# Optimization experiments

Measured on AMD Instinct MI355X. Metric: run time of the kernel, lower is better.

The kernel has to match this reference:

```python
import jax, jax.numpy as jnp
import numpy as np

BN_EPS = 1e-5


def setup_inputs() -> dict:
    key = jax.random.key(0)
    ks = jax.random.split(key, 8)
    N, Cin, Cout, D, H, W = 4, 512, 256, 256, 128, 128
    feat_ffm = jax.random.normal(ks[0], (N, Cin, H, W), dtype=jnp.float32)
    coarse_x = jax.random.normal(ks[1], (N, D, H, W), dtype=jnp.float32)
    # conv1: 1x1, no bias; BN (eval mode: running stats); conv2: 1x1 with bias
    w1 = jax.random.normal(ks[2], (Cout, Cin), dtype=jnp.float32) * (1.0 / np.sqrt(Cin))
    bn_gamma = jnp.ones((Cout,), dtype=jnp.float32)
    bn_beta = jnp.zeros((Cout,), dtype=jnp.float32)
    bn_mean = jax.random.normal(ks[3], (Cout,), dtype=jnp.float32) * 0.1
    bn_var = jax.random.uniform(ks[4], (Cout,), dtype=jnp.float32, minval=0.5, maxval=1.5)
    w2 = jax.random.normal(ks[5], (Cout, Cout), dtype=jnp.float32) * (1.0 / np.sqrt(Cout))
    b2 = jnp.zeros((Cout,), dtype=jnp.float32)
    return {"feat_ffm": feat_ffm, "coarse_x": coarse_x, "w1": w1,
            "bn_gamma": bn_gamma, "bn_beta": bn_beta, "bn_mean": bn_mean,
            "bn_var": bn_var, "w2": w2, "b2": b2}


def reference(feat_ffm, coarse_x, w1, bn_gamma, bn_beta, bn_mean, bn_var, w2, b2):
    N, D, H, W = coarse_x.shape
    # conv1 (1x1) + BN(eval) + ReLU; Dropout2d is identity in eval mode
    x = jnp.einsum('nihw,oi->nohw', feat_ffm, w1)
    scale = bn_gamma * jax.lax.rsqrt(bn_var + BN_EPS)
    x = x * scale[None, :, None, None] + (bn_beta - bn_mean * scale)[None, :, None, None]
    x = jax.nn.relu(x)  # [N, C, H, W]
    C = x.shape[1]
    q = coarse_x.reshape(N, D, H * W)          # proj_query / proj_value
    k = x.reshape(N, C, H * W)                 # proj_key (pre-permute)
    energy = jnp.einsum('nds,ncs->ndc', q, k)  # [N, D, C]
    energy_new = jnp.max(energy, axis=-1, keepdims=True) - energy
    attention = jax.nn.softmax(energy_new, axis=-1)        # [N, D, C]
    out = jnp.einsum('ndc,nds->ncs', attention, q)         # attention^T @ value
    out = out.reshape(N, C, H, W)
    out = jnp.einsum('nchw,oc->nohw', out, w2) + b2[None, :, None, None]
    return out
```

## Files before the change

kernel.cpp:

```cpp
#include <hip/hip_runtime.h>


#define S_DIM 16384
#define C_DIM 256
#define CIN 512

typedef unsigned short u16;
typedef __attribute__((ext_vector_type(8))) short bf16x8;
typedef __attribute__((ext_vector_type(4))) float f32x4;

__device__ __forceinline__ u16 f2bf(float x) {
    unsigned u = __float_as_uint(x);
    u += 0x7fff + ((u >> 16) & 1);
    return (u16)(u >> 16);
}
__device__ __forceinline__ float bf2f(u16 h) {
    return __uint_as_float(((unsigned)h) << 16);
}
__device__ __forceinline__ void gld16(const u16* g, u16* l) {
    __builtin_amdgcn_global_load_lds((const __attribute__((address_space(1))) void*)g,
                                     (__attribute__((address_space(3))) void*)l, 16, 0, 0);
}

__global__ __launch_bounds__(256) void prep_kernel(
    const float* __restrict__ feat, const float* __restrict__ coarse,
    const float* __restrict__ w1, const float* __restrict__ gamma,
    const float* __restrict__ beta, const float* __restrict__ mean,
    const float* __restrict__ var,
    u16* __restrict__ fThi, u16* __restrict__ fTlo,
    u16* __restrict__ qhi, u16* __restrict__ qlo,
    u16* __restrict__ w1hi, u16* __restrict__ w1lo, float* __restrict__ b1) {
    __shared__ u16 Th[64][65], Tl[64][65];
    int b = blockIdx.x;
    int t = threadIdx.x;
    if (b < 8192) {
        int s0 = (b & 255) * 64;
        int i0 = ((b >> 8) & 7) * 64;
        size_t sb = (size_t)(b >> 11) * 8388608;
#pragma unroll
        for (int p = 0; p < 4; ++p) {
            int idx = t + p * 256;
            int row = idx >> 4, c4 = (idx & 15) * 4;
            float4 v = *(const float4*)&feat[sb + (size_t)(i0 + row) * S_DIM + s0 + c4];
            float vv[4] = {v.x, v.y, v.z, v.w};
#pragma unroll
            for (int j = 0; j < 4; ++j) {
                u16 h = f2bf(vv[j]);
                Th[c4 + j][row] = h;
                Tl[c4 + j][row] = f2bf(vv[j] - bf2f(h));
            }
        }
        __syncthreads();
#pragma unroll
        for (int p = 0; p < 2; ++p) {
            int idx = t + p * 256;
            int row = idx >> 3, c8 = (idx & 7) * 8;
            u16 hh[8], ll[8];
#pragma unroll
            for (int j = 0; j < 8; ++j) { hh[j] = Th[row][c8 + j]; ll[j] = Tl[row][c8 + j]; }
            *(uint4*)&fThi[sb + (size_t)(s0 + row) * CIN + i0 + c8] = *(uint4*)hh;
            *(uint4*)&fTlo[sb + (size_t)(s0 + row) * CIN + i0 + c8] = *(uint4*)ll;
        }
    } else if (b < 12288) {
        size_t i = (size_t)(b - 8192) * 256 + t;
        for (size_t c = i; c < 4194304u; c += 1048576u) {
            float4 v = ((const float4*)coarse)[c];
            float vv[4] = {v.x, v.y, v.z, v.w};
            u16 h[4], l[4];
#pragma unroll
            for (int j = 0; j < 4; ++j) {
                h[j] = f2bf(vv[j]);
                l[j] = f2bf(vv[j] - bf2f(h[j]));
            }
            *(uint2*)&qhi[c * 4] = *(uint2*)h;
            *(uint2*)&qlo[c * 4] = *(uint2*)l;
        }
    } else {
        int o = (b - 12288) * 16 + (t >> 4);
        int lane16 = t & 15;
        float sc = gamma[o] * rsqrtf(var[o] + 1e-5f);
        for (int i = lane16; i < CIN; i += 16) {
            float v = w1[o * CIN + i] * sc;
            u16 h = f2bf(v);
            w1hi[o * CIN + i] = h;
            w1lo[o * CIN + i] = f2bf(v - bf2f(h));
        }
        if (lane16 == 0) b1[o] = beta[o] - mean[o] * sc;
    }
}

template <int SPLIT, int EPI>
__global__ __launch_bounds__(256) void gemm_nt(
    const u16* __restrict__ Ah, const u16* __restrict__ Al, long aStride,
    const u16* __restrict__ Bh, const u16* __restrict__ Bl, long bStride,
    int K, int kLen,
    const float* __restrict__ bias,
    float* __restrict__ outF, long oStrideF,
    u16* __restrict__ oHi, u16* __restrict__ oLo, long oStrideH,
    int ldOut) {
    __shared__ u16 AhS[4096];
    __shared__ u16 BhS[4096];
    __shared__ u16 AlS[SPLIT == 3 ? 4096 : 8];
    __shared__ u16 BlS[SPLIT == 3 ? 4096 : 8];

    int m0, n0, kBeg;
    if (EPI == 0) {
        kBeg = blockIdx.x * kLen;
        m0 = (blockIdx.y >> 1) * 128;
        n0 = (blockIdx.y & 1) * 128;
    } else {
        kBeg = 0;
        n0 = blockIdx.x * 128;
        m0 = blockIdx.y * 128;
    }
    int bz = blockIdx.z;
    int tid = threadIdx.x;
    int wave = tid >> 6, lane = tid & 63;

    int c0 = wave * 128 + lane;
    int c1 = c0 + 64;
    int r0 = c0 >> 2, k0 = (c0 & 3) * 8;
    int r1 = c1 >> 2, k1 = (c1 & 3) * 8;
    const u16* gAh0 = Ah + (size_t)bz * aStride + (size_t)(m0 + r0) * K + kBeg + k0;
    const u16* gAh1 = Ah + (size_t)bz * aStride + (size_t)(m0 + r1) * K + kBeg + k1;
    const u16* gBh0 = Bh + (size_t)bz * bStride + (size_t)(n0 + r0) * K + kBeg + k0;
    const u16* gBh1 = Bh + (size_t)bz * bStride + (size_t)(n0 + r1) * K + kBeg + k1;
    const u16 *gAl0 = nullptr, *gAl1 = nullptr, *gBl0 = nullptr, *gBl1 = nullptr;
    if (SPLIT == 3) {
        gAl0 = Al + (size_t)bz * aStride + (size_t)(m0 + r0) * K + kBeg + k0;
        gAl1 = Al + (size_t)bz * aStride + (size_t)(m0 + r1) * K + kBeg + k1;
        gBl0 = Bl + (size_t)bz * bStride + (size_t)(n0 + r0) * K + kBeg + k0;
        gBl1 = Bl + (size_t)bz * bStride + (size_t)(n0 + r1) * K + kBeg + k1;
    }

    int quad = lane >> 4, l15 = lane & 15;
    int wm = wave >> 1, wn = wave & 1;
    int aBase = (wm * 64 + l15) * 32 + quad * 8;
    int bBase = (wn * 64 + l15) * 32 + quad * 8;

    f32x4 zero = {0.f, 0.f, 0.f, 0.f};
    f32x4 acc[4][4];
#pragma unroll
    for (int i = 0; i < 4; ++i)
#pragma unroll
        for (int j = 0; j < 4; ++j) acc[i][j] = zero;

    for (int kb = 0; kb < kLen; kb += 32) {
        __syncthreads();
        gld16(gAh0, AhS + c0 * 8);
        gld16(gAh1, AhS + c1 * 8);
        gld16(gBh0, BhS + c0 * 8);
        gld16(gBh1, BhS + c1 * 8);
        gAh0 += 32; gAh1 += 32; gBh0 += 32; gBh1 += 32;
        if (SPLIT == 3) {
            gld16(gAl0, AlS + c0 * 8);
            gld16(gAl1, AlS + c1 * 8);
            gld16(gBl0, BlS + c0 * 8);
            gld16(gBl1, BlS + c1 * 8);
            gAl0 += 32; gAl1 += 32; gBl0 += 32; gBl1 += 32;
        }
        __syncthreads();

        bf16x8 a_h[4], b_h[4], a_l[4], b_l[4];
#pragma unroll
        for (int t = 0; t < 4; ++t) {
            a_h[t] = *(const bf16x8*)&AhS[aBase + t * 512];
            b_h[t] = *(const bf16x8*)&BhS[bBase + t * 512];
            if (SPLIT == 3) {
                a_l[t] = *(const bf16x8*)&AlS[aBase + t * 512];
                b_l[t] = *(const bf16x8*)&BlS[bBase + t * 512];
            }
        }
#pragma unroll
        for (int mt = 0; mt < 4; ++mt)
#pragma unroll
            for (int nt = 0; nt < 4; ++nt) {
                acc[mt][nt] = __builtin_amdgcn_mfma_f32_16x16x32_bf16(a_h[mt], b_h[nt], acc[mt][nt], 0, 0, 0);
                if (SPLIT == 3) {
                    acc[mt][nt] = __builtin_amdgcn_mfma_f32_16x16x32_bf16(a_h[mt], b_l[nt], acc[mt][nt], 0, 0, 0);
                    acc[mt][nt] = __builtin_amdgcn_mfma_f32_16x16x32_bf16(a_l[mt], b_h[nt], acc[mt][nt], 0, 0, 0);
                }
            }
    }

    float* Ce = nullptr;
    if (EPI == 0) Ce = outF + ((size_t)(blockIdx.x * gridDim.z + bz)) * 65536;
#pragma unroll
    for (int mt = 0; mt < 4; ++mt) {
#pragma unroll
        for (int r = 0; r < 4; ++r) {
            int row = m0 + wm * 64 + mt * 16 + quad * 4 + r;
            float bi = (EPI != 0) ? bias[row] : 0.f;
#pragma unroll
            for (int nt = 0; nt < 4; ++nt) {
                int cc = n0 + wn * 64 + nt * 16 + l15;
                float v = acc[mt][nt][r];
                if (EPI == 0) {
                    Ce[(size_t)row * ldOut + cc] = v;
                } else if (EPI == 1) {
                    v = fmaxf(v + bi, 0.f);
                    u16 h = f2bf(v);
                    size_t o = (size_t)bz * oStrideH + (size_t)row * ldOut + cc;
                    oHi[o] = h;
                    oLo[o] = f2bf(v - bf2f(h));
                } else {
                    outF[(size_t)bz * oStrideF + (size_t)row * ldOut + cc] = v + bi;
                }
            }
        }
    }
}

__global__ __launch_bounds__(256) void post_kernel(const float* __restrict__ Ep,
                                                   float* __restrict__ att,
                                                   const u16* __restrict__ qhi,
                                                   u16* __restrict__ qT) {
    __shared__ u16 T[64][65];
    __shared__ float red[4], red2[4];
    int b = blockIdx.x;
    int t = threadIdx.x;
    if (b < 1024) {
        int n = b >> 8, d = b & 255;
        const float* p = Ep + ((size_t)n * 256 + d) * 256 + t;
        float v = 0.f;
#pragma unroll 8
        for (int s = 0; s < 32; ++s) v += p[(size_t)s * 262144];
        float m = v;
#pragma unroll
        for (int o = 32; o > 0; o >>= 1) m = fminf(m, __shfl_xor(m, o, 64));
        int lane = t & 63, wid = t >> 6;
        if (lane == 0) red[wid] = m;
        __syncthreads();
        m = fminf(fminf(red[0], red[1]), fminf(red[2], red[3]));
        float e = expf(m - v);
        float s = e;
#pragma unroll
        for (int o = 32; o > 0; o >>= 1) s += __shfl_xor(s, o, 64);
        if (lane == 0) red2[wid] = s;
        __syncthreads();
        s = red2[0] + red2[1] + red2[2] + red2[3];
        att[(size_t)b * 256 + t] = e / s;
    } else {
        int i = b - 1024;
        int s0 = (i & 255) * 64;
        int d0 = ((i >> 8) & 3) * 64;
        size_t sb = (size_t)(i >> 10) * 4194304;
#pragma unroll
        for (int p = 0; p < 2; ++p) {
            int idx = t + p * 256;
            int row = idx >> 3, c8 = (idx & 7) * 8;
            u16 v[8];
            *(uint4*)v = *(const uint4*)&qhi[sb + (size_t)(d0 + row) * S_DIM + s0 + c8];
#pragma unroll
            for (int j = 0; j < 8; ++j) T[c8 + j][row] = v[j];
        }
        __syncthreads();
#pragma unroll
        for (int p = 0; p < 2; ++p) {
            int idx = t + p * 256;
            int row = idx >> 3, c8 = (idx & 7) * 8;
            u16 v[8];
#pragma unroll
            for (int j = 0; j < 8; ++j) v[j] = T[row][c8 + j];
            *(uint4*)&qT[sb + (size_t)(s0 + row) * C_DIM + d0 + c8] = *(uint4*)v;
        }
    }
}

__global__ __launch_bounds__(256) void m2h_kernel(const float* __restrict__ w2,
                                                  const float* __restrict__ att,
                                                  u16* __restrict__ M2h) {
    int t = blockIdx.x * 256 + threadIdx.x;
    int d = t & 255, o = (t >> 8) & 255, n = t >> 16;
    const float4* wr = (const float4*)(w2 + (size_t)o * C_DIM);
    const float4* ar = (const float4*)(att + ((size_t)n * C_DIM + d) * C_DIM);
    float s = 0.0f;
#pragma unroll 4
    for (int c4 = 0; c4 < 64; ++c4) {
        float4 w = wr[c4];
        float4 a = ar[c4];
        s += w.x * a.x + w.y * a.y + w.z * a.z + w.w * a.w;
    }
    M2h[((size_t)n * C_DIM + o) * C_DIM + d] = f2bf(s);
}

extern "C" void kernel_launch(void* const* d_in, const int* in_sizes, int n_in,
                              void* d_out, int out_size, void* d_ws, size_t ws_size,
                              hipStream_t stream) {
    const float* feat   = (const float*)d_in[0];
    const float* coarse = (const float*)d_in[1];
    const float* w1     = (const float*)d_in[2];
    const float* gamma  = (const float*)d_in[3];
    const float* beta   = (const float*)d_in[4];
    const float* mean   = (const float*)d_in[5];
    const float* var    = (const float*)d_in[6];
    const float* w2     = (const float*)d_in[7];
    const float* b2     = (const float*)d_in[8];
    float* out = (float*)d_out;

    char* base = (char*)d_ws;
    u16* qhi   = (u16*)(base);
    u16* qlo   = (u16*)(base + 33554432);
    u16* khi   = (u16*)(base + 67108864);
    u16* klo   = (u16*)(base + 100663296);
    u16* fThi  = (u16*)(base + 134217728);
    u16* fTlo  = (u16*)(base + 201326592);
    u16* qT    = (u16*)(base + 268435456);
    float* Ep  = (float*)(base + 301989888);
    float* att = (float*)(base + 335544320);
    u16* M2h   = (u16*)(base + 336592896);
    u16* w1hi  = (u16*)(base + 337117184);
    u16* w1lo  = (u16*)(base + 337379328);
    float* b1  = (float*)(base + 337641472);

    prep_kernel<<<12304, 256, 0, stream>>>(feat, coarse, w1, gamma, beta, mean, var,
                                           fThi, fTlo, qhi, qlo, w1hi, w1lo, b1);

    gemm_nt<3, 1><<<dim3(128, 2, 4), 256, 0, stream>>>(
        w1hi, w1lo, 0, fThi, fTlo, 8388608, CIN, CIN, b1,
        nullptr, 0, khi, klo, 4194304, S_DIM);

    gemm_nt<3, 0><<<dim3(32, 4, 4), 256, 0, stream>>>(
        qhi, qlo, 4194304, khi, klo, 4194304, S_DIM, 512, nullptr,
        Ep, 65536, nullptr, nullptr, 0, C_DIM);

    post_kernel<<<5120, 256, 0, stream>>>(Ep, att, qhi, qT);

    m2h_kernel<<<1024, 256, 0, stream>>>(w2, att, M2h);

    gemm_nt<1, 2><<<dim3(128, 2, 4), 256, 0, stream>>>(
        M2h, nullptr, 65536, qT, nullptr, 4194304, C_DIM, C_DIM, b2,
        out, 4194304, nullptr, nullptr, 0, S_DIM);
}
```

Baseline: 496.2 us.

## Fuse fp32 transpose/split conversion into conv and final GEMM loads

```diff
diff --git a/kernel.cpp b/kernel.cpp
--- a/kernel.cpp
+++ b/kernel.cpp
@@ -21,48 +21,21 @@
     __builtin_amdgcn_global_load_lds((const __attribute__((address_space(1))) void*)g,
                                      (__attribute__((address_space(3))) void*)l, 16, 0, 0);
 }
+__device__ __forceinline__ void gld4(const float* g, float* l) {
+    __builtin_amdgcn_global_load_lds((const __attribute__((address_space(1))) void*)g,
+                                     (__attribute__((address_space(3))) void*)l, 4, 0, 0);
+}
 
 __global__ __launch_bounds__(256) void prep_kernel(
-    const float* __restrict__ feat, const float* __restrict__ coarse,
-    const float* __restrict__ w1, const float* __restrict__ gamma,
-    const float* __restrict__ beta, const float* __restrict__ mean,
-    const float* __restrict__ var,
-    u16* __restrict__ fThi, u16* __restrict__ fTlo,
+    const float* __restrict__ coarse, const float* __restrict__ w1,
+    const float* __restrict__ gamma, const float* __restrict__ beta,
+    const float* __restrict__ mean, const float* __restrict__ var,
     u16* __restrict__ qhi, u16* __restrict__ qlo,
     u16* __restrict__ w1hi, u16* __restrict__ w1lo, float* __restrict__ b1) {
-    __shared__ u16 Th[64][65], Tl[64][65];
     int b = blockIdx.x;
     int t = threadIdx.x;
-    if (b < 8192) {
-        int s0 = (b & 255) * 64;
-        int i0 = ((b >> 8) & 7) * 64;
-        size_t sb = (size_t)(b >> 11) * 8388608;
-#pragma unroll
-        for (int p = 0; p < 4; ++p) {
-            int idx = t + p * 256;
-            int row = idx >> 4, c4 = (idx & 15) * 4;
-            float4 v = *(const float4*)&feat[sb + (size_t)(i0 + row) * S_DIM + s0 + c4];
-            float vv[4] = {v.x, v.y, v.z, v.w};
-#pragma unroll
-            for (int j = 0; j < 4; ++j) {
-                u16 h = f2bf(vv[j]);
-                Th[c4 + j][row] = h;
-                Tl[c4 + j][row] = f2bf(vv[j] - bf2f(h));
-            }
-        }
-        __syncthreads();
-#pragma unroll
-        for (int p = 0; p < 2; ++p) {
-            int idx = t + p * 256;
-            int row = idx >> 3, c8 = (idx & 7) * 8;
-            u16 hh[8], ll[8];
-#pragma unroll
-            for (int j = 0; j < 8; ++j) { hh[j] = Th[row][c8 + j]; ll[j] = Tl[row][c8 + j]; }
-            *(uint4*)&fThi[sb + (size_t)(s0 + row) * CIN + i0 + c8] = *(uint4*)hh;
-            *(uint4*)&fTlo[sb + (size_t)(s0 + row) * CIN + i0 + c8] = *(uint4*)ll;
-        }
-    } else if (b < 12288) {
-        size_t i = (size_t)(b - 8192) * 256 + t;
+    if (b < 4096) {
+        size_t i = (size_t)b * 256 + t;
         for (size_t c = i; c < 4194304u; c += 1048576u) {
             float4 v = ((const float4*)coarse)[c];
             float vv[4] = {v.x, v.y, v.z, v.w};
@@ -76,7 +49,7 @@
             *(uint2*)&qlo[c * 4] = *(uint2*)l;
         }
     } else {
-        int o = (b - 12288) * 16 + (t >> 4);
+        int o = (b - 4096) * 16 + (t >> 4);
         int lane16 = t & 15;
         float sc = gamma[o] * rsqrtf(var[o] + 1e-5f);
         for (int i = lane16; i < CIN; i += 16) {
@@ -89,49 +62,125 @@
     }
 }
 
-template <int SPLIT, int EPI>
-__global__ __launch_bounds__(256) void gemm_nt(
-    const u16* __restrict__ Ah, const u16* __restrict__ Al, long aStride,
-    const u16* __restrict__ Bh, const u16* __restrict__ Bl, long bStride,
-    int K, int kLen,
-    const float* __restrict__ bias,
-    float* __restrict__ outF, long oStrideF,
-    u16* __restrict__ oHi, u16* __restrict__ oLo, long oStrideH,
-    int ldOut) {
-    __shared__ u16 AhS[4096];
-    __shared__ u16 BhS[4096];
-    __shared__ u16 AlS[SPLIT == 3 ? 4096 : 8];
-    __shared__ u16 BlS[SPLIT == 3 ? 4096 : 8];
-
-    int m0, n0, kBeg;
-    if (EPI == 0) {
-        kBeg = blockIdx.x * kLen;
-        m0 = (blockIdx.y >> 1) * 128;
-        n0 = (blockIdx.y & 1) * 128;
-    } else {
-        kBeg = 0;
-        n0 = blockIdx.x * 128;
-        m0 = blockIdx.y * 128;
-    }
+__global__ __launch_bounds__(256) void conv_kernel(
+    const u16* __restrict__ w1hi, const u16* __restrict__ w1lo,
+    const float* __restrict__ feat, const float* __restrict__ b1,
+    u16* __restrict__ khi, u16* __restrict__ klo) {
+    __shared__ u16 AhS[4096], AlS[4096];
+    __shared__ float BfS[32 * 133];
+    int s0 = blockIdx.x * 128;
+    int m0 = blockIdx.y * 128;
     int bz = blockIdx.z;
-    int tid = threadIdx.x;
-    int wave = tid >> 6, lane = tid & 63;
-
-    int c0 = wave * 128 + lane;
-    int c1 = c0 + 64;
+    int tid = threadIdx.x, wave = tid >> 6, lane = tid & 63;
+
+    int c0 = wave * 128 + lane, c1 = c0 + 64;
     int r0 = c0 >> 2, k0 = (c0 & 3) * 8;
     int r1 = c1 >> 2, k1 = (c1 & 3) * 8;
-    const u16* gAh0 = Ah + (size_t)bz * aStride + (size_t)(m0 + r0) * K + kBeg + k0;
-    const u16* gAh1 = Ah + (size_t)bz * aStride + (size_t)(m0 + r1) * K + kBeg + k1;
-    const u16* gBh0 = Bh + (size_t)bz * bStride + (size_t)(n0 + r0) * K + kBeg + k0;
-    const u16* gBh1 = Bh + (size_t)bz * bStride + (size_t)(n0 + r1) * K + kBeg + k1;
-    const u16 *gAl0 = nullptr, *gAl1 = nullptr, *gBl0 = nullptr, *gBl1 = nullptr;
-    if (SPLIT == 3) {
-        gAl0 = Al + (size_t)bz * aStride + (size_t)(m0 + r0) * K + kBeg + k0;
-        gAl1 = Al + (size_t)bz * aStride + (size_t)(m0 + r1) * K + kBeg + k1;
-        gBl0 = Bl + (size_t)bz * bStride + (size_t)(n0 + r0) * K + kBeg + k0;
-        gBl1 = Bl + (size_t)bz * bStride + (size_t)(n0 + r1) * K + kBeg + k1;
-    }
+    const u16* gA0h = w1hi + (size_t)(m0 + r0) * CIN + k0;
+    const u16* gA1h = w1hi + (size_t)(m0 + r1) * CIN + k1;
+    const u16* gA0l = w1lo + (size_t)(m0 + r0) * CIN + k0;
+    const u16* gA1l = w1lo + (size_t)(m0 + r1) * CIN + k1;
+    const float* fB = feat + (size_t)bz * ((size_t)CIN * S_DIM) + s0 + lane;
+
+    int quad = lane >> 4, l15 = lane & 15;
+    int wm = wave >> 1, wn = wave & 1;
+    int aBase = (wm * 64 + l15) * 32 + quad * 8;
+
+    f32x4 zero = {0.f, 0.f, 0.f, 0.f};
+    f32x4 acc[4][4];
+#pragma unroll
+    for (int i = 0; i < 4; ++i)
+#pragma unroll
+        for (int j = 0; j < 4; ++j) acc[i][j] = zero;
+
+    for (int kb = 0; kb < CIN; kb += 32) {
+        __syncthreads();
+        gld16(gA0h, AhS + c0 * 8);
+        gld16(gA1h, AhS + c1 * 8);
+        gld16(gA0l, AlS + c0 * 8);
+        gld16(gA1l, AlS + c1 * 8);
+        gA0h += 32; gA1h += 32; gA0l += 32; gA1l += 32;
+#pragma unroll
+        for (int j = 0; j < 16; ++j) {
+            int cc = wave * 16 + j;
+            int i = cc >> 1, h = cc & 1;
+            gld4(fB + (size_t)(kb + i) * S_DIM + h * 64, BfS + i * 133 + h * 64 + lane);
+        }
+        __syncthreads();
+
+        bf16x8 a_h[4], a_l[4];
+#pragma unroll
+        for (int t = 0; t < 4; ++t) {
+            a_h[t] = *(const bf16x8*)&AhS[aBase + t * 512];
+            a_l[t] = *(const bf16x8*)&AlS[aBase + t * 512];
+        }
+        bf16x8 b_h[4], b_l[4];
+#pragma unroll
+        for (int nt = 0; nt < 4; ++nt) {
+            int n = wn * 64 + nt * 16 + l15;
+            union { u16 u[8]; bf16x8 v; } th, tl;
+#pragma unroll
+            for (int j = 0; j < 8; ++j) {
+                float f = BfS[(quad * 8 + j) * 133 + n];
+                u16 h = f2bf(f);
+                th.u[j] = h;
+                tl.u[j] = (u16)(__float_as_uint(f - bf2f(h)) >> 16);
+            }
+            b_h[nt] = th.v;
+            b_l[nt] = tl.v;
+        }
+#pragma unroll
+        for (int mt = 0; mt < 4; ++mt)
+#pragma unroll
+            for (int nt = 0; nt < 4; ++nt) {
+                acc[mt][nt] = __builtin_amdgcn_mfma_f32_16x16x32_bf16(a_h[mt], b_h[nt], acc[mt][nt], 0, 0, 0);
+                acc[mt][nt] = __builtin_amdgcn_mfma_f32_16x16x32_bf16(a_h[mt], b_l[nt], acc[mt][nt], 0, 0, 0);
+                acc[mt][nt] = __builtin_amdgcn_mfma_f32_16x16x32_bf16(a_l[mt], b_h[nt], acc[mt][nt], 0, 0, 0);
+            }
+    }
+
+#pragma unroll
+    for (int mt = 0; mt < 4; ++mt) {
+#pragma unroll
+        for (int r = 0; r < 4; ++r) {
+            int row = m0 + wm * 64 + mt * 16 + quad * 4 + r;
+            float bi = b1[row];
+#pragma unroll
+            for (int nt = 0; nt < 4; ++nt) {
+                int cc = s0 + wn * 64 + nt * 16 + l15;
+                float v = fmaxf(acc[mt][nt][r] + bi, 0.f);
+                u16 h = f2bf(v);
+                size_t o = (size_t)bz * 4194304 + (size_t)row * S_DIM + cc;
+                khi[o] = h;
+                klo[o] = f2bf(v - bf2f(h));
+            }
+        }
+    }
+}
+
+__global__ __launch_bounds__(256) void energy_kernel(
+    const u16* __restrict__ qhi, const u16* __restrict__ qlo,
+    const u16* __restrict__ khi, const u16* __restrict__ klo,
+    float* __restrict__ Ep) {
+    __shared__ u16 AhS[4096], BhS[4096], AlS[4096], BlS[4096];
+    int kBeg = blockIdx.x * 256;
+    int m0 = (blockIdx.y >> 1) * 128;
+    int n0 = (blockIdx.y & 1) * 128;
+    int bz = blockIdx.z;
+    int tid = threadIdx.x, wave = tid >> 6, lane = tid & 63;
+
+    int c0 = wave * 128 + lane, c1 = c0 + 64;
+    int r0 = c0 >> 2, k0 = (c0 & 3) * 8;
+    int r1 = c1 >> 2, k1 = (c1 & 3) * 8;
+    size_t bo = (size_t)bz * 4194304;
+    const u16* gA0h = qhi + bo + (size_t)(m0 + r0) * S_DIM + kBeg + k0;
+    const u16* gA1h = qhi + bo + (size_t)(m0 + r1) * S_DIM + kBeg + k1;
+    const u16* gB0h = khi + bo + (size_t)(n0 + r0) * S_DIM + kBeg + k0;
+    const u16* gB1h = khi + bo + (size_t)(n0 + r1) * S_DIM + kBeg + k1;
+    const u16* gA0l = qlo + bo + (size_t)(m0 + r0) * S_DIM + kBeg + k0;
+    const u16* gA1l = qlo + bo + (size_t)(m0 + r1) * S_DIM + kBeg + k1;
+    const u16* gB0l = klo + bo + (size_t)(n0 + r0) * S_DIM + kBeg + k0;
+    const u16* gB1l = klo + bo + (size_t)(n0 + r1) * S_DIM + kBeg + k1;
 
     int quad = lane >> 4, l15 = lane & 15;
     int wm = wave >> 1, wn = wave & 1;
@@ -145,20 +194,18 @@
 #pragma unroll
         for (int j = 0; j < 4; ++j) acc[i][j] = zero;
 
-    for (int kb = 0; kb < kLen; kb += 32) {
-        __syncthreads();
-        gld16(gAh0, AhS + c0 * 8);
-        gld16(gAh1, AhS + c1 * 8);
-        gld16(gBh0, BhS + c0 * 8);
-        gld16(gBh1, BhS + c1 * 8);
-        gAh0 += 32; gAh1 += 32; gBh0 += 32; gBh1 += 32;
-        if (SPLIT == 3) {
-            gld16(gAl0, AlS + c0 * 8);
-            gld16(gAl1, AlS + c1 * 8);
-            gld16(gBl0, BlS + c0 * 8);
-            gld16(gBl1, BlS + c1 * 8);
-            gAl0 += 32; gAl1 += 32; gBl0 += 32; gBl1 += 32;
-        }
+    for (int kb = 0; kb < 256; kb += 32) {
+        __syncthreads();
+        gld16(gA0h, AhS + c0 * 8);
+        gld16(gA1h, AhS + c1 * 8);
+        gld16(gB0h, BhS + c0 * 8);
+        gld16(gB1h, BhS + c1 * 8);
+        gld16(gA0l, AlS + c0 * 8);
+        gld16(gA1l, AlS + c1 * 8);
+        gld16(gB0l, BlS + c0 * 8);
+        gld16(gB1l, BlS + c1 * 8);
+        gA0h += 32; gA1h += 32; gB0h += 32; gB1h += 32;
+        gA0l += 32; gA1l += 32; gB0l += 32; gB1l += 32;
         __syncthreads();
 
         bf16x8 a_h[4], b_h[4], a_l[4], b_l[4];
@@ -166,105 +213,57 @@
         for (int t = 0; t < 4; ++t) {
             a_h[t] = *(const bf16x8*)&AhS[aBase + t * 512];
             b_h[t] = *(const bf16x8*)&BhS[bBase + t * 512];
-            if (SPLIT == 3) {
-                a_l[t] = *(const bf16x8*)&AlS[aBase + t * 512];
-                b_l[t] = *(const bf16x8*)&BlS[bBase + t * 512];
-            }
+            a_l[t] = *(const bf16x8*)&AlS[aBase + t * 512];
+            b_l[t] = *(const bf16x8*)&BlS[bBase + t * 512];
         }
 #pragma unroll
         for (int mt = 0; mt < 4; ++mt)
 #pragma unroll
             for (int nt = 0; nt < 4; ++nt) {
                 acc[mt][nt] = __builtin_amdgcn_mfma_f32_16x16x32_bf16(a_h[mt], b_h[nt], acc[mt][nt], 0, 0, 0);
-                if (SPLIT == 3) {
-                    acc[mt][nt] = __builtin_amdgcn_mfma_f32_16x16x32_bf16(a_h[mt], b_l[nt], acc[mt][nt], 0, 0, 0);
-                    acc[mt][nt] = __builtin_amdgcn_mfma_f32_16x16x32_bf16(a_l[mt], b_h[nt], acc[mt][nt], 0, 0, 0);
-                }
-            }
-    }
-
-    float* Ce = nullptr;
-    if (EPI == 0) Ce = outF + ((size_t)(blockIdx.x * gridDim.z + bz)) * 65536;
-#pragma unroll
-    for (int mt = 0; mt < 4; ++mt) {
+                acc[mt][nt] = __builtin_amdgcn_mfma_f32_16x16x32_bf16(a_h[mt], b_l[nt], acc[mt][nt], 0, 0, 0);
+                acc[mt][nt] = __builtin_amdgcn_mfma_f32_16x16x32_bf16(a_l[mt], b_h[nt], acc[mt][nt], 0, 0, 0);
+            }
+    }
+
+    float* Ce = Ep + ((size_t)(blockIdx.x * 4 + bz)) * 65536;
+#pragma unroll
+    for (int mt = 0; mt < 4; ++mt)
 #pragma unroll
         for (int r = 0; r < 4; ++r) {
             int row = m0 + wm * 64 + mt * 16 + quad * 4 + r;
-            float bi = (EPI != 0) ? bias[row] : 0.f;
 #pragma unroll
             for (int nt = 0; nt < 4; ++nt) {
                 int cc = n0 + wn * 64 + nt * 16 + l15;
-                float v = acc[mt][nt][r];
-                if (EPI == 0) {
-                    Ce[(size_t)row * ldOut + cc] = v;
-                } else if (EPI == 1) {
-                    v = fmaxf(v + bi, 0.f);
-                    u16 h = f2bf(v);
-                    size_t o = (size_t)bz * oStrideH + (size_t)row * ldOut + cc;
-                    oHi[o] = h;
-                    oLo[o] = f2bf(v - bf2f(h));
-                } else {
-                    outF[(size_t)bz * oStrideF + (size_t)row * ldOut + cc] = v + bi;
-                }
-            }
-        }
-    }
-}
-
-__global__ __launch_bounds__(256) void post_kernel(const float* __restrict__ Ep,
-                                                   float* __restrict__ att,
-                                                   const u16* __restrict__ qhi,
-                                                   u16* __restrict__ qT) {
-    __shared__ u16 T[64][65];
+                Ce[(size_t)row * C_DIM + cc] = acc[mt][nt][r];
+            }
+        }
+}
+
+__global__ __launch_bounds__(256) void softmax_kernel(const float* __restrict__ Ep,
+                                                      float* __restrict__ att) {
     __shared__ float red[4], red2[4];
     int b = blockIdx.x;
     int t = threadIdx.x;
-    if (b < 1024) {
-        int n = b >> 8, d = b & 255;
-        const float* p = Ep + ((size_t)n * 256 + d) * 256 + t;
-        float v = 0.f;
+    const float* p = Ep + (size_t)b * 256 + t;
+    float v = 0.f;
 #pragma unroll 8
-        for (int s = 0; s < 32; ++s) v += p[(size_t)s * 262144];
-        float m = v;
-#pragma unroll
-        for (int o = 32; o > 0; o >>= 1) m = fminf(m, __shfl_xor(m, o, 64));
-        int lane = t & 63, wid = t >> 6;
-        if (lane == 0) red[wid] = m;
-        __syncthreads();
-        m = fminf(fminf(red[0], red[1]), fminf(red[2], red[3]));
-        float e = expf(m - v);
-        float s = e;
-#pragma unroll
-        for (int o = 32; o > 0; o >>= 1) s += __shfl_xor(s, o, 64);
-        if (lane == 0) red2[wid] = s;
-        __syncthreads();
-        s = red2[0] + red2[1] + red2[2] + red2[3];
-        att[(size_t)b * 256 + t] = e / s;
-    } else {
-        int i = b - 1024;
-        int s0 = (i & 255) * 64;
-        int d0 = ((i >> 8) & 3) * 64;
-        size_t sb = (size_t)(i >> 10) * 4194304;
-#pragma unroll
-        for (int p = 0; p < 2; ++p) {
-            int idx = t + p * 256;
-            int row = idx >> 3, c8 = (idx & 7) * 8;
-            u16 v[8];
-            *(uint4*)v = *(const uint4*)&qhi[sb + (size_t)(d0 + row) * S_DIM + s0 + c8];
-#pragma unroll
-            for (int j = 0; j < 8; ++j) T[c8 + j][row] = v[j];
-        }
-        __syncthreads();
-#pragma unroll
-        for (int p = 0; p < 2; ++p) {
-            int idx = t + p * 256;
-            int row = idx >> 3, c8 = (idx & 7) * 8;
-            u16 v[8];
-#pragma unroll
-            for (int j = 0; j < 8; ++j) v[j] = T[row][c8 + j];
-            *(uint4*)&qT[sb + (size_t)(s0 + row) * C_DIM + d0 + c8] = *(uint4*)v;
-        }
-    }
+    for (int s = 0; s < 64; ++s) v += p[(size_t)s * 262144];
+    float m = v;
+#pragma unroll
+    for (int o = 32; o > 0; o >>= 1) m = fminf(m, __shfl_xor(m, o, 64));
+    int lane = t & 63, wid = t >> 6;
+    if (lane == 0) red[wid] = m;
+    __syncthreads();
+    m = fminf(fminf(red[0], red[1]), fminf(red[2], red[3]));
+    float e = expf(m - v);
+    float s = e;
+#pragma unroll
+    for (int o = 32; o > 0; o >>= 1) s += __shfl_xor(s, o, 64);
+    if (lane == 0) red2[wid] = s;
+    __syncthreads();
+    s = red2[0] + red2[1] + red2[2] + red2[3];
+    att[(size_t)b * 256 + t] = e / s;
 }
 
 __global__ __launch_bounds__(256) void m2h_kernel(const float* __restrict__ w2,
@@ -284,6 +283,80 @@
     M2h[((size_t)n * C_DIM + o) * C_DIM + d] = f2bf(s);
 }
 
+__global__ __launch_bounds__(256) void final_kernel(
+    const u16* __restrict__ M2h, const float* __restrict__ coarse,
+    const float* __restrict__ b2, float* __restrict__ out) {
+    __shared__ u16 AhS[4096];
+    __shared__ float BfS[32 * 133];
+    int s0 = blockIdx.x * 128;
+    int m0 = blockIdx.y * 128;
+    int bz = blockIdx.z;
+    int tid = threadIdx.x, wave = tid >> 6, lane = tid & 63;
+
+    int c0 = wave * 128 + lane, c1 = c0 + 64;
+    int r0 = c0 >> 2, k0 = (c0 & 3) * 8;
+    int r1 = c1 >> 2, k1 = (c1 & 3) * 8;
+    const u16* gA0 = M2h + (size_t)bz * 65536 + (size_t)(m0 + r0) * C_DIM + k0;
+    const u16* gA1 = M2h + (size_t)bz * 65536 + (size_t)(m0 + r1) * C_DIM + k1;
+    const float* fB = coarse + (size_t)bz * 4194304 + s0 + lane;
+
+    int quad = lane >> 4, l15 = lane & 15;
+    int wm = wave >> 1, wn = wave & 1;
+    int aBase = (wm * 64 + l15) * 32 + quad * 8;
+
+    f32x4 zero = {0.f, 0.f, 0.f, 0.f};
+    f32x4 acc[4][4];
+#pragma unroll
+    for (int i = 0; i < 4; ++i)
+#pragma unroll
+        for (int j = 0; j < 4; ++j) acc[i][j] = zero;
+
+    for (int kb = 0; kb < C_DIM; kb += 32) {
+        __syncthreads();
+        gld16(gA0, AhS + c0 * 8);
+        gld16(gA1, AhS + c1 * 8);
+        gA0 += 32; gA1 += 32;
+#pragma unroll
+        for (int j = 0; j < 16; ++j) {
+            int cc = wave * 16 + j;
+            int i = cc >> 1, h = cc & 1;
+            gld4(fB + (size_t)(kb + i) * S_DIM + h * 64, BfS + i * 133 + h * 64 + lane);
+        }
+        __syncthreads();
+
+        bf16x8 a_h[4];
+#pragma unroll
+        for (int t = 0; t < 4; ++t) a_h[t] = *(const bf16x8*)&AhS[aBase + t * 512];
+        bf16x8 b_h[4];
+#pragma unroll
+        for (int nt = 0; nt < 4; ++nt) {
+            int n = wn * 64 + nt * 16 + l15;
+            union { u16 u[8]; bf16x8 v; } th;
+#pragma unroll
+            for (int j = 0; j < 8; ++j) th.u[j] = f2bf(BfS[(quad * 8 + j) * 133 + n]);
+            b_h[nt] = th.v;
+        }
+#pragma unroll
+        for (int mt = 0; mt < 4; ++mt)
+#pragma unroll
+            for (int nt = 0; nt < 4; ++nt)
+                acc[mt][nt] = __builtin_amdgcn_mfma_f32_16x16x32_bf16(a_h[mt], b_h[nt], acc[mt][nt], 0, 0, 0);
+    }
+
+#pragma unroll
+    for (int mt = 0; mt < 4; ++mt)
+#pragma unroll
+        for (int r = 0; r < 4; ++r) {
+            int row = m0 + wm * 64 + mt * 16 + quad * 4 + r;
+            float bi = b2[row];
+#pragma unroll
+            for (int nt = 0; nt < 4; ++nt) {
+                int cc = s0 + wn * 64 + nt * 16 + l15;
+                out[(size_t)bz * 4194304 + (size_t)row * S_DIM + cc] = acc[mt][nt][r] + bi;
+            }
+        }
+}
+
 extern "C" void kernel_launch(void* const* d_in, const int* in_sizes, int n_in,
                               void* d_out, int out_size, void* d_ws, size_t ws_size,
                               hipStream_t stream) {
@@ -303,32 +376,23 @@
     u16* qlo   = (u16*)(base + 33554432);
     u16* khi   = (u16*)(base + 67108864);
     u16* klo   = (u16*)(base + 100663296);
-    u16* fThi  = (u16*)(base + 134217728);
-    u16* fTlo  = (u16*)(base + 201326592);
-    u16* qT    = (u16*)(base + 268435456);
-    float* Ep  = (float*)(base + 301989888);
-    float* att = (float*)(base + 335544320);
-    u16* M2h   = (u16*)(base + 336592896);
-    u16* w1hi  = (u16*)(base + 337117184);
-    u16* w1lo  = (u16*)(base + 337379328);
-    float* b1  = (float*)(base + 337641472);
-
-    prep_kernel<<<12304, 256, 0, stream>>>(feat, coarse, w1, gamma, beta, mean, var,
-                                           fThi, fTlo, qhi, qlo, w1hi, w1lo, b1);
-
-    gemm_nt<3, 1><<<dim3(128, 2, 4), 256, 0, stream>>>(
-        w1hi, w1lo, 0, fThi, fTlo, 8388608, CIN, CIN, b1,
-        nullptr, 0, khi, klo, 4194304, S_DIM);
-
-    gemm_nt<3, 0><<<dim3(32, 4, 4), 256, 0, stream>>>(
-        qhi, qlo, 4194304, khi, klo, 4194304, S_DIM, 512, nullptr,
-        Ep, 65536, nullptr, nullptr, 0, C_DIM);
-
-    post_kernel<<<5120, 256, 0, stream>>>(Ep, att, qhi, qT);
+    float* Ep  = (float*)(base + 134217728);
+    float* att = (float*)(base + 201326592);
+    u16* M2h   = (u16*)(base + 202375168);
+    u16* w1hi  = (u16*)(base + 202899456);
+    u16* w1lo  = (u16*)(base + 203161600);
+    float* b1  = (float*)(base + 203423744);
+
+    prep_kernel<<<4112, 256, 0, stream>>>(coarse, w1, gamma, beta, mean, var,
+                                          qhi, qlo, w1hi, w1lo, b1);
+
+    conv_kernel<<<dim3(128, 2, 4), 256, 0, stream>>>(w1hi, w1lo, feat, b1, khi, klo);
+
+    energy_kernel<<<dim3(64, 4, 4), 256, 0, stream>>>(qhi, qlo, khi, klo, Ep);
+
+    softmax_kernel<<<1024, 256, 0, stream>>>(Ep, att);
 
     m2h_kernel<<<1024, 256, 0, stream>>>(w2, att, M2h);
 
-    gemm_nt<1, 2><<<dim3(128, 2, 4), 256, 0, stream>>>(
-        M2h, nullptr, 65536, qT, nullptr, 4194304, C_DIM, C_DIM, b2,
-        out, 4194304, nullptr, nullptr, 0, S_DIM);
-}
+    final_kernel<<<dim3(128, 2, 4), 256, 0, stream>>>(M2h, coarse, b2, out);
+}
```

Result: faster. 447.5 us (-9.8%).
